# Kernel tuning notes

Measured on AMD Instinct MI355X. Metric: run time of the kernel, lower is better.

Reference implementation:

```python
import jax, jax.numpy as jnp
import numpy as np

N = 50000
E = 1600000
D_IN = 128
D_HID = 128
K = 16  # n_clusters


def spmm(edge_index, edge_weight, feats):
    # out[i] = sum_{(i<-j) in edges} w_e * feats[j]
    dst, src = edge_index[0], edge_index[1]
    msgs = feats[src] * edge_weight[:, None]  # [E, d]
    return jax.ops.segment_sum(msgs, dst, num_segments=N)


def gcn_with_skip(x, edge_index, edge_weight, W, b, skip_w):
    transformed = x @ W + b                      # Linear kernel
    propagated = spmm(edge_index, edge_weight, transformed)
    return jax.nn.selu(skip_w * transformed + propagated)


def setup_inputs() -> dict:
    key = jax.random.key(0)
    ks = jax.random.split(key, 12)
    x = jax.random.normal(ks[0], (N, D_IN), dtype=jnp.float32)
    edge_index = jax.random.randint(ks[1], (2, E), 0, N, dtype=jnp.int32)
    edge_weight = jax.random.uniform(ks[2], (E,), dtype=jnp.float32)
    s1 = 1.0 / np.sqrt(D_IN)
    s2 = 1.0 / np.sqrt(D_HID)
    W1 = jax.random.uniform(ks[3], (D_IN, D_HID), jnp.float32, -s1, s1)
    b1 = jax.random.uniform(ks[4], (D_HID,), jnp.float32, -s1, s1)
    skip1 = jnp.ones((D_HID,), jnp.float32)
    W2 = jax.random.uniform(ks[5], (D_HID, D_HID), jnp.float32, -s2, s2)
    b2 = jax.random.uniform(ks[6], (D_HID,), jnp.float32, -s2, s2)
    skip2 = jnp.ones((D_HID,), jnp.float32)
    Wa = jax.random.uniform(ks[7], (D_HID, K), jnp.float32, -s2, s2)
    ba = jax.random.uniform(ks[8], (K,), jnp.float32, -s2, s2)
    return {"x": x, "edge_index": edge_index, "edge_weight": edge_weight,
            "W1": W1, "b1": b1, "skip1": skip1,
            "W2": W2, "b2": b2, "skip2": skip2,
            "Wa": Wa, "ba": ba}


def reference(x, edge_index, edge_weight, W1, b1, skip1, W2, b2, skip2, Wa, ba):
    h = gcn_with_skip(x, edge_index, edge_weight, W1, b1, skip1)
    h = gcn_with_skip(h, edge_index, edge_weight, W2, b2, skip2)
    assignments = jax.nn.softmax(h @ Wa + ba, axis=-1)  # [N, K]
    return assignments
```

## Files before the change

kernel.cpp:

```cpp
#include <hip/hip_runtime.h>
#include <hip/hip_bf16.h>
#include <hip/hip_fp16.h>

#define NN 50000
#define NE 1600000
#define DD 128
#define KC 16

#define NB 3125
#define CHUNK 6144
#define NCHUNK 261
#define BT 512
#define EPT 12
#define MAXB 768
#define SB 772

#define G1B 196
#define ZBLK 13
#define HB_LD 136

typedef __attribute__((ext_vector_type(8))) short s8v;
typedef __attribute__((ext_vector_type(4))) float f4v;
typedef __attribute__((ext_vector_type(2))) float f2v;

#define FMIXW_LO(a, wf, pk) \
    asm("v_fma_mix_f32 %0, %1, %2, %0 op_sel:[0,0,0] op_sel_hi:[0,1,0]" \
        : "+v"(a) : "v"(wf), "v"(pk))
#define FMIXW_HI(a, wf, pk) \
    asm("v_fma_mix_f32 %0, %1, %2, %0 op_sel:[0,1,0] op_sel_hi:[0,1,0]" \
        : "+v"(a) : "v"(wf), "v"(pk))

__device__ __forceinline__ f2v uph2(unsigned u) {
    __half2 h = *reinterpret_cast<__half2*>(&u);
    f2v r;
    r.x = __low2float(h);
    r.y = __high2float(h);
    return r;
}


__device__ __forceinline__ void wprep_one(const float* __restrict__ W, s8v* __restrict__ Wf, int g) {
    int l = g & 63;
    int kcnt = g >> 6;
    int kc = kcnt >> 3, nt = kcnt & 7;
    int n = nt * 16 + (l & 15);
    int kb = kc * 32 + (l >> 4) * 8;
    union { s8v v; __hip_bfloat162 h2[4]; } u;
    #pragma unroll
    for (int q = 0; q < 4; q++) {
        float lo = W[(size_t)(kb + 2 * q) * 128 + n];
        float hi = W[(size_t)(kb + 2 * q + 1) * 128 + n];
        u.h2[q] = __float22bfloat162_rn(make_float2(lo, hi));
    }
    Wf[(size_t)kcnt * 64 + l] = u.v;
}


__global__ __launch_bounds__(256) void k_init(int* __restrict__ gcur,
                                              const float* __restrict__ W1,
                                              const float* __restrict__ W2,
                                              s8v* __restrict__ Wf1,
                                              s8v* __restrict__ Wf2) {
    int bid = blockIdx.x, t = threadIdx.x;
    if (bid < ZBLK) {
        int i = bid * 256 + t;
        if (i < NB) gcur[i] = 0;
        return;
    }
    int wb = bid - ZBLK;
    if (wb < 8) wprep_one(W1, Wf1, wb * 256 + t);
    else        wprep_one(W2, Wf2, (wb - 8) * 256 + t);
}


__device__ __forceinline__ s8v load_afrag(const float* p) {
    union { s8v v; __hip_bfloat162 h2[4]; } a;
    float4 f0 = *(const float4*)p;
    float4 f1 = *(const float4*)(p + 4);
    a.h2[0] = __float22bfloat162_rn(make_float2(f0.x, f0.y));
    a.h2[1] = __float22bfloat162_rn(make_float2(f0.z, f0.w));
    a.h2[2] = __float22bfloat162_rn(make_float2(f1.x, f1.y));
    a.h2[3] = __float22bfloat162_rn(make_float2(f1.z, f1.w));
    return a.v;
}

__device__ __forceinline__ void gemm_body(const float* __restrict__ X,
                                          const s8v* __restrict__ Wf,
                                          const float* __restrict__ bias,
                                          __half* __restrict__ Out,
                                          int nrows, int wave, int lane) {
    int m0 = wave * 32;
    if (m0 >= nrows) return;
    int col = lane & 15;
    int quad = lane >> 4;

    f4v acc[2][8];
    #pragma unroll
    for (int mt = 0; mt < 2; mt++)
        #pragma unroll
        for (int nt = 0; nt < 8; nt++) acc[mt][nt] = (f4v){0.f, 0.f, 0.f, 0.f};

    int row0 = m0 + col;
    int row1 = m0 + 16 + col;
    if (row0 >= nrows) row0 = nrows - 1;
    if (row1 >= nrows) row1 = nrows - 1;
    const float* xr0 = X + (size_t)row0 * 128 + quad * 8;
    const float* xr1 = X + (size_t)row1 * 128 + quad * 8;

    #pragma unroll 1
    for (int kc = 0; kc < 4; kc++) {
        s8v a0 = load_afrag(xr0 + kc * 32);
        s8v a1 = load_afrag(xr1 + kc * 32);
        #pragma unroll
        for (int nt = 0; nt < 8; nt++) {
            s8v b = Wf[(size_t)(kc * 8 + nt) * 64 + lane];
            acc[0][nt] = __builtin_amdgcn_mfma_f32_16x16x32_bf16(a0, b, acc[0][nt], 0, 0, 0);
            acc[1][nt] = __builtin_amdgcn_mfma_f32_16x16x32_bf16(a1, b, acc[1][nt], 0, 0, 0);
        }
    }

    float bb[8];
    #pragma unroll
    for (int nt = 0; nt < 8; nt++) bb[nt] = bias[nt * 16 + col];

    #pragma unroll
    for (int mt = 0; mt < 2; mt++) {
        #pragma unroll
        for (int r = 0; r < 4; r++) {
            int row = m0 + mt * 16 + quad * 4 + r;
            if (row < nrows) {
                __half* orow = Out + (size_t)row * 128 + col;
                #pragma unroll
                for (int nt = 0; nt < 8; nt++) {
                    orow[nt * 16] = __float2half(acc[mt][nt][r] + bb[nt]);
                }
            }
        }
    }
}


__global__ __launch_bounds__(BT) void k_binprep(const int* __restrict__ dst,
                                                const int* __restrict__ src,
                                                const float* __restrict__ w,
                                                int2* __restrict__ staging,
                                                int* __restrict__ gcur,
                                                const float* __restrict__ x,
                                                const s8v* __restrict__ Wf1,
                                                const float* __restrict__ b1,
                                                __half* __restrict__ T) {
    __shared__ int cnt[NB];
    int t = threadIdx.x;
    int bid = blockIdx.x;

    if (bid >= NCHUNK) {
        int wave = (bid - NCHUNK) * 8 + (t >> 6);
        gemm_body(x, Wf1, b1, T, NN, wave, t & 63);
        return;
    }

    int c = bid;
    size_t cbase = (size_t)c * CHUNK;
    for (int i = t; i < NB; i += BT) cnt[i] = 0;
    __syncthreads();

    int dreg[EPT], sreg[EPT]; float wreg[EPT];
    #pragma unroll
    for (int j = 0; j < EPT; j++) {
        size_t e = cbase + j * BT + t;
        bool ok = e < NE;
        size_t ee = ok ? e : (NE - 1);
        dreg[j] = dst[ee]; sreg[j] = src[ee]; wreg[j] = w[ee];
        if (!ok) dreg[j] = -1;
        if (ok) atomicAdd(&cnt[dreg[j] >> 4], 1);
    }
    __syncthreads();

    for (int i = t; i < NB; i += BT) {
        int cc = cnt[i];
        if (cc > 0) cnt[i] = atomicAdd(&gcur[i], cc);
    }
    __syncthreads();

    #pragma unroll
    for (int j = 0; j < EPT; j++) {
        if (dreg[j] >= 0) {
            int b = dreg[j] >> 4;
            int pos = atomicAdd(&cnt[b], 1);
            if (pos < MAXB)
                staging[(size_t)b * SB + pos] =
                    make_int2(sreg[j] | ((dreg[j] & 15) << 16), __float_as_int(wreg[j]));
        }
    }
}


template <int MODE>
__global__ __launch_bounds__(256) void k_spmm(const __half* __restrict__ T,
                                              const int2* __restrict__ staging,
                                              const int* __restrict__ gcur,
                                              const float* __restrict__ skip,
                                              const s8v* __restrict__ Wfb,
                                              const float* __restrict__ bias2,
                                              __half* __restrict__ T2,
                                              const float* __restrict__ Wa,
                                              const float* __restrict__ ba,
                                              float* __restrict__ aout) {
    __shared__ __align__(16) int2 srec[MAXB + 8];
    __shared__ int rcnt[16];
    __shared__ int rowoff[17];
    __shared__ __align__(16) __hip_bfloat16 hbuf[(MODE == 0) ? (16 * HB_LD) : 8];
    int b = blockIdx.x;
    int tid = threadIdx.x;
    int wv = tid >> 6, lane = tid & 63;
    int q = lane >> 4;
    int fk = lane & 15;

    int cnt = gcur[b];
    if (cnt > MAXB) cnt = MAXB;

    if (tid < 16) rcnt[tid] = 0;
    __syncthreads();

    const int2* gp = staging + (size_t)b * SB;
    int i0 = tid, i1 = tid + 256, i2 = tid + 512;
    bool h0 = i0 < cnt, h1 = i1 < cnt, h2 = i2 < cnt;
    int2 mr0, mr1, mr2;
    if (h0) { mr0 = gp[i0]; atomicAdd(&rcnt[(unsigned)mr0.x >> 16], 1); }
    if (h1) { mr1 = gp[i1]; atomicAdd(&rcnt[(unsigned)mr1.x >> 16], 1); }
    if (h2) { mr2 = gp[i2]; atomicAdd(&rcnt[(unsigned)mr2.x >> 16], 1); }
    __syncthreads();

    if (tid < 16) {
        int vv = rcnt[tid];
        int p = vv;
        #pragma unroll
        for (int off = 1; off < 16; off <<= 1) {
            int u = __shfl_up(p, off, 64);
            if (tid >= off) p += u;
        }
        rowoff[tid] = p - vv;
        if (tid == 15) rowoff[16] = p;
        rcnt[tid] = p - vv;
    }
    __syncthreads();

    if (h0) { int p = atomicAdd(&rcnt[(unsigned)mr0.x >> 16], 1); srec[p] = mr0; }
    if (h1) { int p = atomicAdd(&rcnt[(unsigned)mr1.x >> 16], 1); srec[p] = mr1; }
    if (h2) { int p = atomicAdd(&rcnt[(unsigned)mr2.x >> 16], 1); srec[p] = mr2; }
    if (tid < 8) srec[cnt + tid] = make_int2(0, 0);
    __syncthreads();

    const char* Tb = (const char*)T;
    unsigned foff = (unsigned)fk << 4;

    float sk[8];
    *(float4*)&sk[0] = *(const float4*)(skip + fk * 8);
    *(float4*)&sk[4] = *(const float4*)(skip + fk * 8 + 4);

    float wreg[32];
    float bav[4];
    if (MODE == 1) {
        #pragma unroll
        for (int j = 0; j < 8; j++)
            *(float4*)&wreg[j * 4] = *(const float4*)(Wa + (size_t)(8 * fk + j) * KC + 4 * q);
        #pragma unroll
        for (int c = 0; c < 4; c++) bav[c] = ba[4 * q + c];
    }

    const float scale = 1.0507009873554805f, alpha = 1.6732632423543772f;

    for (int r = wv; r < 16; r += 4) {
        int g = b * 16 + r;
        int o = rowoff[r], oe = rowoff[r + 1];
        float ac[8];
        #pragma unroll
        for (int j = 0; j < 8; j++) ac[j] = 0.f;

        #define LDT(rc) (*(const int4*)(Tb + (((unsigned)(rc).x & 0xFFFFu) * 256u + foff)))
        #define EDGE(rc, t4)                                               \
            do {                                                           \
                float wf_ = __int_as_float((rc).y);                        \
                FMIXW_LO(ac[0], wf_, (t4).x); FMIXW_HI(ac[1], wf_, (t4).x);\
                FMIXW_LO(ac[2], wf_, (t4).y); FMIXW_HI(ac[3], wf_, (t4).y);\
                FMIXW_LO(ac[4], wf_, (t4).z); FMIXW_HI(ac[5], wf_, (t4).z);\
                FMIXW_LO(ac[6], wf_, (t4).w); FMIXW_HI(ac[7], wf_, (t4).w);\
            } while (0)

        for (; o + 32 <= oe; o += 32) {
            int2 r0 = srec[o + q],      r1 = srec[o + 4 + q];
            int2 r2 = srec[o + 8 + q],  r3 = srec[o + 12 + q];
            int2 r4 = srec[o + 16 + q], r5 = srec[o + 20 + q];
            int2 r6 = srec[o + 24 + q], r7 = srec[o + 28 + q];
            int4 t0 = LDT(r0); int4 t1 = LDT(r1); int4 t2 = LDT(r2); int4 t3 = LDT(r3);
            int4 t4 = LDT(r4); int4 t5 = LDT(r5); int4 t6 = LDT(r6); int4 t7 = LDT(r7);
            EDGE(r0, t0); EDGE(r1, t1); EDGE(r2, t2); EDGE(r3, t3);
            EDGE(r4, t4); EDGE(r5, t5); EDGE(r6, t6); EDGE(r7, t7);
        }
        for (; o + 16 <= oe; o += 16) {
            int2 r0 = srec[o + q],     r1 = srec[o + 4 + q];
            int2 r2 = srec[o + 8 + q], r3 = srec[o + 12 + q];
            int4 t0 = LDT(r0); int4 t1 = LDT(r1); int4 t2 = LDT(r2); int4 t3 = LDT(r3);
            EDGE(r0, t0); EDGE(r1, t1); EDGE(r2, t2); EDGE(r3, t3);
        }
        for (; o + 8 <= oe; o += 8) {
            int2 r0 = srec[o + q], r1 = srec[o + 4 + q];
            int4 t0 = LDT(r0); int4 t1 = LDT(r1);
            EDGE(r0, t0); EDGE(r1, t1);
        }
        for (; o < oe; o += 4) {
            int i = o + q;
            int2 r0 = (i < oe) ? srec[i] : make_int2(0, 0);
            int4 t0 = LDT(r0);
            EDGE(r0, t0);
        }
        #undef EDGE
        #undef LDT

        #pragma unroll
        for (int j = 0; j < 8; j++) {
            ac[j] += __shfl_xor(ac[j], 16, 64);
            ac[j] += __shfl_xor(ac[j], 32, 64);
        }

        int4 ts = *(const int4*)(Tb + ((unsigned)g * 256u + foff));
        f2v s01 = uph2(ts.x), s23 = uph2(ts.y), s45 = uph2(ts.z), s67 = uph2(ts.w);
        float v[8];
        v[0] = sk[0] * s01.x + ac[0]; v[1] = sk[1] * s01.y + ac[1];
        v[2] = sk[2] * s23.x + ac[2]; v[3] = sk[3] * s23.y + ac[3];
        v[4] = sk[4] * s45.x + ac[4]; v[5] = sk[5] * s45.y + ac[5];
        v[6] = sk[6] * s67.x + ac[6]; v[7] = sk[7] * s67.y + ac[7];
        #pragma unroll
        for (int j = 0; j < 8; j++)
            v[j] = scale * (v[j] > 0.f ? v[j] : alpha * (__expf(v[j]) - 1.f));

        if (MODE == 0) {
            if (q == 0) {
                union { int4 i4; __hip_bfloat162 h2[4]; } pk;
                #pragma unroll
                for (int j = 0; j < 4; j++)
                    pk.h2[j] = __float22bfloat162_rn(make_float2(v[2 * j], v[2 * j + 1]));
                *(int4*)&hbuf[r * HB_LD + fk * 8] = pk.i4;
            }
        } else {
            float p4[4] = {0.f, 0.f, 0.f, 0.f};
            #pragma unroll
            for (int j = 0; j < 8; j++)
                #pragma unroll
                for (int c = 0; c < 4; c++) p4[c] += v[j] * wreg[j * 4 + c];
            #pragma unroll
            for (int off = 1; off <= 8; off <<= 1)
                #pragma unroll
                for (int c = 0; c < 4; c++) p4[c] += __shfl_xor(p4[c], off, 64);
            #pragma unroll
            for (int c = 0; c < 4; c++) p4[c] += bav[c];
            float m = fmaxf(fmaxf(p4[0], p4[1]), fmaxf(p4[2], p4[3]));
            m = fmaxf(m, __shfl_xor(m, 16, 64));
            m = fmaxf(m, __shfl_xor(m, 32, 64));
            float e0 = __expf(p4[0] - m), e1 = __expf(p4[1] - m);
            float e2 = __expf(p4[2] - m), e3 = __expf(p4[3] - m);
            float s = e0 + e1 + e2 + e3;
            s += __shfl_xor(s, 16, 64);
            s += __shfl_xor(s, 32, 64);
            if (fk < 4) {
                float ev = e0;
                ev = (fk == 1) ? e1 : ev;
                ev = (fk == 2) ? e2 : ev;
                ev = (fk == 3) ? e3 : ev;
                aout[(size_t)g * KC + 4 * q + fk] = ev / s;
            }
        }
    }

    if (MODE == 0) {
        __syncthreads();
        int col = fk;
        int quad = q;
        int nt0 = wv * 2, nt1 = nt0 + 1;
        f4v acc0 = (f4v){0.f, 0.f, 0.f, 0.f};
        f4v acc1 = (f4v){0.f, 0.f, 0.f, 0.f};
        #pragma unroll
        for (int kc = 0; kc < 4; kc++) {
            s8v a = *(const s8v*)&hbuf[col * HB_LD + kc * 32 + quad * 8];
            s8v b0 = Wfb[(size_t)(kc * 8 + nt0) * 64 + lane];
            s8v b1 = Wfb[(size_t)(kc * 8 + nt1) * 64 + lane];
            acc0 = __builtin_amdgcn_mfma_f32_16x16x32_bf16(a, b0, acc0, 0, 0, 0);
            acc1 = __builtin_amdgcn_mfma_f32_16x16x32_bf16(a, b1, acc1, 0, 0, 0);
        }
        float bb0 = bias2[nt0 * 16 + col];
        float bb1 = bias2[nt1 * 16 + col];
        #pragma unroll
        for (int r4 = 0; r4 < 4; r4++) {
            int grow = b * 16 + quad * 4 + r4;
            __half* orow = T2 + (size_t)grow * 128;
            orow[nt0 * 16 + col] = __float2half(acc0[r4] + bb0);
            orow[nt1 * 16 + col] = __float2half(acc1[r4] + bb1);
        }
    }
}


extern "C" void kernel_launch(void* const* d_in, const int* in_sizes, int n_in,
                              void* d_out, int out_size, void* d_ws, size_t ws_size,
                              hipStream_t stream) {
    const float* x     = (const float*)d_in[0];
    const int*   eidx  = (const int*)d_in[1];
    const float* ew    = (const float*)d_in[2];
    const float* W1    = (const float*)d_in[3];
    const float* b1    = (const float*)d_in[4];
    const float* skip1 = (const float*)d_in[5];
    const float* W2    = (const float*)d_in[6];
    const float* b2    = (const float*)d_in[7];
    const float* skip2 = (const float*)d_in[8];
    const float* Wa    = (const float*)d_in[9];
    const float* ba    = (const float*)d_in[10];
    float* out = (float*)d_out;

    const int* dst = eidx;
    const int* src = eidx + NE;

    char* ws = (char*)d_ws;
    size_t off = 0;
    __half* T  = (__half*)(ws + off);                 off += (size_t)NN * DD * 2;
    __half* T2 = (__half*)(ws + off);                 off += (size_t)NN * DD * 2;
    int2* staging = (int2*)(ws + off);                off += (size_t)NB * SB * 8;
    int* gcur = (int*)(ws + off);                     off += (size_t)NB * 4 + 1024;
    s8v* Wf1 = (s8v*)(ws + off);                      off += 2048 * 16;
    s8v* Wf2 = (s8v*)(ws + off);                      off += 2048 * 16;

    k_init<<<ZBLK + 16, 256, 0, stream>>>(gcur, W1, W2, Wf1, Wf2);
    k_binprep<<<NCHUNK + G1B, BT, 0, stream>>>(dst, src, ew, staging, gcur,
                                               x, Wf1, b1, T);
    k_spmm<0><<<NB, 256, 0, stream>>>(T, staging, gcur, skip1,
                                      Wf2, b2, T2, nullptr, nullptr, nullptr);
    k_spmm<1><<<NB, 256, 0, stream>>>(T2, staging, gcur, skip2,
                                      nullptr, nullptr, nullptr, Wa, ba, out);
}
```

Before: 243.8 us.

## Pack edge records into 32 bits with quantized weights and reuse sorted rows

Edge records shrink from 8 to 4 bytes by packing the source index, the row-within-bin and a 12-bit fixed-point weight, with the scale applied once after accumulation. The first SpMM pass writes its per-bin row-sorted records and row offsets back to global memory, so the second pass loads them directly and skips the atomic counting sort. This cuts staging memory traffic and second-layer setup work. The cost is weight quantization error and an extra write in the first pass.

```diff
diff --git a/kernel.cpp b/kernel.cpp
--- a/kernel.cpp
+++ b/kernel.cpp
@@ -13,7 +13,8 @@
 #define BT 512
 #define EPT 12
 #define MAXB 768
-#define SB 772
+#define SB4 776
+#define INV4096 2.44140625e-4f
 
 #define G1B 196
 #define ZBLK 13
@@ -143,7 +144,7 @@
 __global__ __launch_bounds__(BT) void k_binprep(const int* __restrict__ dst,
                                                 const int* __restrict__ src,
                                                 const float* __restrict__ w,
-                                                int2* __restrict__ staging,
+                                                unsigned* __restrict__ staging4,
                                                 int* __restrict__ gcur,
                                                 const float* __restrict__ x,
                                                 const s8v* __restrict__ Wf1,
@@ -187,9 +188,11 @@
         if (dreg[j] >= 0) {
             int b = dreg[j] >> 4;
             int pos = atomicAdd(&cnt[b], 1);
+            unsigned wq = (unsigned)__float2int_rn(wreg[j] * 4096.f);
+            if (wq > 4095u) wq = 4095u;
             if (pos < MAXB)
-                staging[(size_t)b * SB + pos] =
-                    make_int2(sreg[j] | ((dreg[j] & 15) << 16), __float_as_int(wreg[j]));
+                staging4[(size_t)b * SB4 + pos] =
+                    (unsigned)sreg[j] | ((unsigned)(dreg[j] & 15) << 16) | (wq << 20);
         }
     }
 }
@@ -197,8 +200,9 @@
 
 template <int MODE>
 __global__ __launch_bounds__(256) void k_spmm(const __half* __restrict__ T,
-                                              const int2* __restrict__ staging,
+                                              unsigned* __restrict__ staging4,
                                               const int* __restrict__ gcur,
+                                              int* __restrict__ rowptr,
                                               const float* __restrict__ skip,
                                               const s8v* __restrict__ Wfb,
                                               const float* __restrict__ bias2,
@@ -206,7 +210,7 @@
                                               const float* __restrict__ Wa,
                                               const float* __restrict__ ba,
                                               float* __restrict__ aout) {
-    __shared__ __align__(16) int2 srec[MAXB + 8];
+    __shared__ __align__(16) unsigned srec[MAXB + 8];
     __shared__ int rcnt[16];
     __shared__ int rowoff[17];
     __shared__ __align__(16) __hip_bfloat16 hbuf[(MODE == 0) ? (16 * HB_LD) : 8];
@@ -216,40 +220,48 @@
     int q = lane >> 4;
     int fk = lane & 15;
 
-    int cnt = gcur[b];
-    if (cnt > MAXB) cnt = MAXB;
-
-    if (tid < 16) rcnt[tid] = 0;
-    __syncthreads();
-
-    const int2* gp = staging + (size_t)b * SB;
-    int i0 = tid, i1 = tid + 256, i2 = tid + 512;
-    bool h0 = i0 < cnt, h1 = i1 < cnt, h2 = i2 < cnt;
-    int2 mr0, mr1, mr2;
-    if (h0) { mr0 = gp[i0]; atomicAdd(&rcnt[(unsigned)mr0.x >> 16], 1); }
-    if (h1) { mr1 = gp[i1]; atomicAdd(&rcnt[(unsigned)mr1.x >> 16], 1); }
-    if (h2) { mr2 = gp[i2]; atomicAdd(&rcnt[(unsigned)mr2.x >> 16], 1); }
-    __syncthreads();
-
-    if (tid < 16) {
-        int vv = rcnt[tid];
-        int p = vv;
-        #pragma unroll
-        for (int off = 1; off < 16; off <<= 1) {
-            int u = __shfl_up(p, off, 64);
-            if (tid >= off) p += u;
-        }
-        rowoff[tid] = p - vv;
-        if (tid == 15) rowoff[16] = p;
-        rcnt[tid] = p - vv;
-    }
-    __syncthreads();
-
-    if (h0) { int p = atomicAdd(&rcnt[(unsigned)mr0.x >> 16], 1); srec[p] = mr0; }
-    if (h1) { int p = atomicAdd(&rcnt[(unsigned)mr1.x >> 16], 1); srec[p] = mr1; }
-    if (h2) { int p = atomicAdd(&rcnt[(unsigned)mr2.x >> 16], 1); srec[p] = mr2; }
-    if (tid < 8) srec[cnt + tid] = make_int2(0, 0);
-    __syncthreads();
+    if (MODE == 0) {
+        int cnt = gcur[b];
+        if (cnt > MAXB) cnt = MAXB;
+        if (tid < 16) rcnt[tid] = 0;
+        __syncthreads();
+        unsigned* gp = staging4 + (size_t)b * SB4;
+        int i0 = tid, i1 = tid + 256, i2 = tid + 512;
+        bool h0 = i0 < cnt, h1 = i1 < cnt, h2 = i2 < cnt;
+        unsigned mr0, mr1, mr2;
+        if (h0) { mr0 = gp[i0]; atomicAdd(&rcnt[(mr0 >> 16) & 15], 1); }
+        if (h1) { mr1 = gp[i1]; atomicAdd(&rcnt[(mr1 >> 16) & 15], 1); }
+        if (h2) { mr2 = gp[i2]; atomicAdd(&rcnt[(mr2 >> 16) & 15], 1); }
+        __syncthreads();
+        if (tid < 16) {
+            int vv = rcnt[tid];
+            int p = vv;
+            #pragma unroll
+            for (int off = 1; off < 16; off <<= 1) {
+                int u = __shfl_up(p, off, 64);
+                if (tid >= off) p += u;
+            }
+            rowoff[tid] = p - vv;
+            if (tid == 15) rowoff[16] = p;
+            rcnt[tid] = p - vv;
+        }
+        __syncthreads();
+        if (h0) { int p = atomicAdd(&rcnt[(mr0 >> 16) & 15], 1); srec[p] = mr0; }
+        if (h1) { int p = atomicAdd(&rcnt[(mr1 >> 16) & 15], 1); srec[p] = mr1; }
+        if (h2) { int p = atomicAdd(&rcnt[(mr2 >> 16) & 15], 1); srec[p] = mr2; }
+        if (tid < 8) srec[cnt + tid] = 0u;
+        __syncthreads();
+        for (int i = tid; i < cnt + 8; i += 256) gp[i] = srec[i];
+        if (tid < 17) rowptr[b * 17 + tid] = rowoff[tid];
+    } else {
+        if (tid < 17) rowoff[tid] = rowptr[b * 17 + tid];
+        __syncthreads();
+        int cnt = rowoff[16];
+        int nv4 = (cnt + 11) >> 2;
+        const uint4* sp4 = (const uint4*)(staging4 + (size_t)b * SB4);
+        for (int i = tid; i < nv4; i += 256) ((uint4*)srec)[i] = sp4[i];
+        __syncthreads();
+    }
 
     const char* Tb = (const char*)T;
     unsigned foff = (unsigned)fk << 4;
@@ -277,10 +289,10 @@
         #pragma unroll
         for (int j = 0; j < 8; j++) ac[j] = 0.f;
 
-        #define LDT(rc) (*(const int4*)(Tb + (((unsigned)(rc).x & 0xFFFFu) * 256u + foff)))
+        #define LDT(rc) (*(const int4*)(Tb + (((rc) & 0xFFFFu) * 256u + foff)))
         #define EDGE(rc, t4)                                               \
             do {                                                           \
-                float wf_ = __int_as_float((rc).y);                        \
+                float wf_ = (float)((rc) >> 20);                           \
                 FMIXW_LO(ac[0], wf_, (t4).x); FMIXW_HI(ac[1], wf_, (t4).x);\
                 FMIXW_LO(ac[2], wf_, (t4).y); FMIXW_HI(ac[3], wf_, (t4).y);\
                 FMIXW_LO(ac[4], wf_, (t4).z); FMIXW_HI(ac[5], wf_, (t4).z);\
@@ -288,29 +300,29 @@
             } while (0)
 
         for (; o + 32 <= oe; o += 32) {
-            int2 r0 = srec[o + q],      r1 = srec[o + 4 + q];
-            int2 r2 = srec[o + 8 + q],  r3 = srec[o + 12 + q];
-            int2 r4 = srec[o + 16 + q], r5 = srec[o + 20 + q];
-            int2 r6 = srec[o + 24 + q], r7 = srec[o + 28 + q];
+            unsigned r0 = srec[o + q],      r1 = srec[o + 4 + q];
+            unsigned r2 = srec[o + 8 + q],  r3 = srec[o + 12 + q];
+            unsigned r4 = srec[o + 16 + q], r5 = srec[o + 20 + q];
+            unsigned r6 = srec[o + 24 + q], r7 = srec[o + 28 + q];
             int4 t0 = LDT(r0); int4 t1 = LDT(r1); int4 t2 = LDT(r2); int4 t3 = LDT(r3);
             int4 t4 = LDT(r4); int4 t5 = LDT(r5); int4 t6 = LDT(r6); int4 t7 = LDT(r7);
             EDGE(r0, t0); EDGE(r1, t1); EDGE(r2, t2); EDGE(r3, t3);
             EDGE(r4, t4); EDGE(r5, t5); EDGE(r6, t6); EDGE(r7, t7);
         }
         for (; o + 16 <= oe; o += 16) {
-            int2 r0 = srec[o + q],     r1 = srec[o + 4 + q];
-            int2 r2 = srec[o + 8 + q], r3 = srec[o + 12 + q];
+            unsigned r0 = srec[o + q],     r1 = srec[o + 4 + q];
+            unsigned r2 = srec[o + 8 + q], r3 = srec[o + 12 + q];
             int4 t0 = LDT(r0); int4 t1 = LDT(r1); int4 t2 = LDT(r2); int4 t3 = LDT(r3);
             EDGE(r0, t0); EDGE(r1, t1); EDGE(r2, t2); EDGE(r3, t3);
         }
         for (; o + 8 <= oe; o += 8) {
-            int2 r0 = srec[o + q], r1 = srec[o + 4 + q];
+            unsigned r0 = srec[o + q], r1 = srec[o + 4 + q];
             int4 t0 = LDT(r0); int4 t1 = LDT(r1);
             EDGE(r0, t0); EDGE(r1, t1);
         }
         for (; o < oe; o += 4) {
             int i = o + q;
-            int2 r0 = (i < oe) ? srec[i] : make_int2(0, 0);
+            unsigned r0 = (i < oe) ? srec[i] : 0u;
             int4 t0 = LDT(r0);
             EDGE(r0, t0);
         }
@@ -326,10 +338,14 @@
         int4 ts = *(const int4*)(Tb + ((unsigned)g * 256u + foff));
         f2v s01 = uph2(ts.x), s23 = uph2(ts.y), s45 = uph2(ts.z), s67 = uph2(ts.w);
         float v[8];
-        v[0] = sk[0] * s01.x + ac[0]; v[1] = sk[1] * s01.y + ac[1];
-        v[2] = sk[2] * s23.x + ac[2]; v[3] = sk[3] * s23.y + ac[3];
-        v[4] = sk[4] * s45.x + ac[4]; v[5] = sk[5] * s45.y + ac[5];
-        v[6] = sk[6] * s67.x + ac[6]; v[7] = sk[7] * s67.y + ac[7];
+        v[0] = fmaf(ac[0], INV4096, sk[0] * s01.x);
+        v[1] = fmaf(ac[1], INV4096, sk[1] * s01.y);
+        v[2] = fmaf(ac[2], INV4096, sk[2] * s23.x);
+        v[3] = fmaf(ac[3], INV4096, sk[3] * s23.y);
+        v[4] = fmaf(ac[4], INV4096, sk[4] * s45.x);
+        v[5] = fmaf(ac[5], INV4096, sk[5] * s45.y);
+        v[6] = fmaf(ac[6], INV4096, sk[6] * s67.x);
+        v[7] = fmaf(ac[7], INV4096, sk[7] * s67.y);
         #pragma unroll
         for (int j = 0; j < 8; j++)
             v[j] = scale * (v[j] > 0.f ? v[j] : alpha * (__expf(v[j]) - 1.f));
@@ -423,16 +439,17 @@
     size_t off = 0;
     __half* T  = (__half*)(ws + off);                 off += (size_t)NN * DD * 2;
     __half* T2 = (__half*)(ws + off);                 off += (size_t)NN * DD * 2;
-    int2* staging = (int2*)(ws + off);                off += (size_t)NB * SB * 8;
+    unsigned* staging4 = (unsigned*)(ws + off);       off += (size_t)NB * SB4 * 4;
     int* gcur = (int*)(ws + off);                     off += (size_t)NB * 4 + 1024;
+    int* rowptr = (int*)(ws + off);                   off += (size_t)NB * 17 * 4;
     s8v* Wf1 = (s8v*)(ws + off);                      off += 2048 * 16;
     s8v* Wf2 = (s8v*)(ws + off);                      off += 2048 * 16;
 
     k_init<<<ZBLK + 16, 256, 0, stream>>>(gcur, W1, W2, Wf1, Wf2);
-    k_binprep<<<NCHUNK + G1B, BT, 0, stream>>>(dst, src, ew, staging, gcur,
+    k_binprep<<<NCHUNK + G1B, BT, 0, stream>>>(dst, src, ew, staging4, gcur,
                                                x, Wf1, b1, T);
-    k_spmm<0><<<NB, 256, 0, stream>>>(T, staging, gcur, skip1,
+    k_spmm<0><<<NB, 256, 0, stream>>>(T, staging4, gcur, rowptr, skip1,
                                       Wf2, b2, T2, nullptr, nullptr, nullptr);
-    k_spmm<1><<<NB, 256, 0, stream>>>(T2, staging, gcur, skip2,
+    k_spmm<1><<<NB, 256, 0, stream>>>(T2, staging4, gcur, rowptr, skip2,
                                       nullptr, nullptr, nullptr, Wa, ba, out);
 }
```

Measured after the change: 236.7 us. 1.03x faster.
